# Optimization experiments

Measured on AMD Instinct MI355X. Metric: run time of the kernel, lower is better.

The kernel has to match this reference:

```python
import jax, jax.numpy as jnp
import numpy as np

NUM_HEADS = 16
HEAD_DIM = 64
EMBED_DIM = NUM_HEADS * HEAD_DIM  # 1024


def setup_inputs() -> dict:
    key = jax.random.key(0)
    k1, k2, k3 = jax.random.split(key, 3)
    B, T, C = 4, 2048, EMBED_DIM
    x = jax.random.normal(k1, (B, T, C), dtype=jnp.float32)
    # Linear weights stored [in, out] so y = x @ W (== torch x @ W.T with torch layout)
    w_qkv = jax.random.normal(k2, (C, 3 * C), dtype=jnp.float32) * (1.0 / np.sqrt(C))
    w_out = jax.random.normal(k3, (C, C), dtype=jnp.float32) * (1.0 / np.sqrt(C))
    return {"x": x, "w_qkv": w_qkv, "w_out": w_out}


def reference(x, w_qkv, w_out):
    B, T, C = x.shape
    H, D = NUM_HEADS, HEAD_DIM
    scale = 1.0 / jnp.sqrt(jnp.asarray(D, dtype=x.dtype))

    qkv = x @ w_qkv  # [B, T, 3C]
    q, k, v = jnp.split(qkv, 3, axis=-1)

    def split_heads(t):
        return t.reshape(B, T, H, D).transpose(0, 2, 1, 3)  # [B, H, T, D]

    q, k, v = split_heads(q), split_heads(k), split_heads(v)

    scores = jnp.einsum("bhqd,bhkd->bhqk", q, k) * scale  # [B, H, T, T]
    causal = jnp.tril(jnp.ones((T, T), dtype=bool))
    scores = jnp.where(causal, scores, -jnp.inf)
    weights = jax.nn.softmax(scores, axis=-1)
    out = jnp.einsum("bhqk,bhkd->bhqd", weights, v)  # [B, H, T, D]
    out = out.transpose(0, 2, 1, 3).reshape(B, T, C)
    return out @ w_out
```

## Files before the change

kernel.cpp:

```cpp
#include <hip/hip_runtime.h>

typedef __attribute__((ext_vector_type(8))) short bf16x8;
typedef __attribute__((ext_vector_type(4))) float f32x4;
typedef __attribute__((ext_vector_type(8))) unsigned short u16x8;

#define USHORT unsigned short

__device__ __forceinline__ USHORT f2bf(float f){
  unsigned int u = __builtin_bit_cast(unsigned int, f);
  u = (u + 0x7FFFu + ((u >> 16) & 1u)) >> 16;
  return (USHORT)u;
}

__device__ __forceinline__ void gl_lds16(const void* g, void* l){
  __builtin_amdgcn_global_load_lds((const __attribute__((address_space(1))) void*)g,
                                   (__attribute__((address_space(3))) void*)l, 16, 0, 0);
}

__global__ __launch_bounds__(256) void cvt_x(const float* __restrict__ x,
                                             USHORT* __restrict__ xb){
  int i = blockIdx.x * 256 + threadIdx.x;
  const float4* p = (const float4*)x;
  float4 a = p[i*2], b = p[i*2+1];
  u16x8 v;
  v[0]=f2bf(a.x); v[1]=f2bf(a.y); v[2]=f2bf(a.z); v[3]=f2bf(a.w);
  v[4]=f2bf(b.x); v[5]=f2bf(b.y); v[6]=f2bf(b.z); v[7]=f2bf(b.w);
  ((u16x8*)xb)[i] = v;
}

__global__ __launch_bounds__(256) void transpose_f32_bf16(const float* __restrict__ src,
                                                          USHORT* __restrict__ dst,
                                                          int rows, int cols){
  __shared__ USHORT t[32][33];
  int x0 = blockIdx.x * 32, y0 = blockIdx.y * 32;
  int tx = threadIdx.x, ty = threadIdx.y;
  #pragma unroll
  for (int i=0;i<4;i++)
    t[ty+i*8][tx] = f2bf(src[(size_t)(y0+ty+i*8)*cols + x0+tx]);
  __syncthreads();
  #pragma unroll
  for (int i=0;i<4;i++)
    dst[(size_t)(x0+ty+i*8)*rows + y0+tx] = t[tx][ty+i*8];
}

__global__ __launch_bounds__(256) void transpose_v(const USHORT* __restrict__ V,
                                                   USHORT* __restrict__ VT){
  __shared__ USHORT t[32][33];
  int bh = blockIdx.z;
  const USHORT* src = V + (size_t)bh*2048*64;
  USHORT* dst = VT + (size_t)bh*64*2048;
  int x0 = blockIdx.x * 32;
  int y0 = blockIdx.y * 32;
  int tx = threadIdx.x, ty = threadIdx.y;
  #pragma unroll
  for (int i=0;i<4;i++)
    t[ty+i*8][tx] = src[(size_t)(y0+ty+i*8)*64 + x0+tx];
  __syncthreads();
  #pragma unroll
  for (int i=0;i<4;i++)
    dst[(size_t)(x0+ty+i*8)*2048 + y0+tx] = t[tx][ty+i*8];
}

template<int EPI>
__global__ __launch_bounds__(256) void gemm_bt(
    const USHORT* __restrict__ A, const USHORT* __restrict__ Bt,
    float* __restrict__ Cf,
    USHORT* __restrict__ Qo, USHORT* __restrict__ Ko, USHORT* __restrict__ Vo,
    int M, int N, int K)
{
  __shared__ USHORT As[128*32];
  __shared__ USHORT Bs[128*32];
  const int tid = threadIdx.x;
  const int lane = tid & 63, li = lane & 15, g = lane >> 4;
  const int wv = tid >> 6, wr = wv >> 1, wc = wv & 1;
  const int m0 = blockIdx.y * 128, n0 = blockIdx.x * 128;

  f32x4 acc[4][4];
  #pragma unroll
  for (int m=0;m<4;m++)
    #pragma unroll
    for (int n=0;n<4;n++) acc[m][n] = (f32x4){0.f,0.f,0.f,0.f};

  for (int kk = 0; kk < K; kk += 32){
    __syncthreads();
    #pragma unroll
    for (int it=0; it<2; ++it){
      int c = it*256 + tid;
      int row = c >> 2, sl = c & 3;
      gl_lds16(A  + (size_t)(m0+row)*K + kk + sl*8, &As[c*8]);
      gl_lds16(Bt + (size_t)(n0+row)*K + kk + sl*8, &Bs[c*8]);
    }
    __syncthreads();
    bf16x8 af[4], bfr[4];
    #pragma unroll
    for (int m=0;m<4;m++) af[m]  = *(const bf16x8*)&As[(wr*64+m*16+li)*32 + g*8];
    #pragma unroll
    for (int n=0;n<4;n++) bfr[n] = *(const bf16x8*)&Bs[(wc*64+n*16+li)*32 + g*8];
    #pragma unroll
    for (int m=0;m<4;m++)
      #pragma unroll
      for (int n=0;n<4;n++)
        acc[m][n] = __builtin_amdgcn_mfma_f32_16x16x32_bf16(af[m], bfr[n], acc[m][n], 0,0,0);
  }

  if (EPI == 0){
    #pragma unroll
    for (int m=0;m<4;m++)
      #pragma unroll
      for (int n=0;n<4;n++){
        int col  = n0 + wc*64 + n*16 + li;
        int rowb = m0 + wr*64 + m*16 + g*4;
        #pragma unroll
        for (int r=0;r<4;r++)
          Cf[(size_t)(rowb+r)*N + col] = acc[m][n][r];
      }
  } else {
    #pragma unroll
    for (int m=0;m<4;m++)
      #pragma unroll
      for (int n=0;n<4;n++){
        int col = n0 + wc*64 + n*16 + li;
        int which = col >> 10, hd = col & 1023, h = hd >> 6, d = hd & 63;
        USHORT* dst = (which==0) ? Qo : ((which==1) ? Ko : Vo);
        float sc = (which==0) ? 0.125f : 1.0f;
        int rowb = m0 + wr*64 + m*16 + g*4;
        #pragma unroll
        for (int r=0;r<4;r++){
          int grow = rowb + r;
          int b = grow >> 11, t = grow & 2047;
          dst[((size_t)(b*16+h)*2048 + t)*64 + d] = f2bf(acc[m][n][r]*sc);
        }
      }
  }
}

__global__ __launch_bounds__(256) void attn_kern(
    const USHORT* __restrict__ Q, const USHORT* __restrict__ Kc,
    const USHORT* __restrict__ VT, USHORT* __restrict__ Aout)
{
  __shared__ USHORT Kl[128*64];
  __shared__ USHORT Vl[64*128];
  __shared__ USHORT Pl[128*128];
  const int qt = blockIdx.x, bh = blockIdx.y;
  const int q0 = qt * 128;
  const int tid = threadIdx.x, lane = tid & 63, li = lane & 15, g = lane >> 4;
  const int wv = tid >> 6;
  const USHORT* Qb = Q  + (size_t)bh*2048*64;
  const USHORT* Kb = Kc + (size_t)bh*2048*64;
  const USHORT* Vb = VT + (size_t)bh*64*2048;

  bf16x8 aq[2][2];
  #pragma unroll
  for (int m=0;m<2;m++)
    #pragma unroll
    for (int ks=0;ks<2;ks++){
      int row = q0 + wv*32 + m*16 + li;
      aq[m][ks] = *(const bf16x8*)&Qb[(size_t)row*64 + ks*32 + g*8];
    }

  f32x4 o[2][4];
  float mrun[2][4], lrun[2][4];
  #pragma unroll
  for (int m=0;m<2;m++){
    #pragma unroll
    for (int n=0;n<4;n++) o[m][n] = (f32x4){0.f,0.f,0.f,0.f};
    #pragma unroll
    for (int r=0;r<4;r++){ mrun[m][r] = -1e30f; lrun[m][r] = 0.f; }
  }

  const int nkt = qt + 1;
  for (int kt = 0; kt < nkt; ++kt){
    __syncthreads();
    #pragma unroll
    for (int it=0; it<4; ++it){
      int c = it*256 + tid;
      { int row = c >> 3, sl = c & 7, gs = sl ^ (row & 7);
        gl_lds16(Kb + ((size_t)(kt*128+row))*64 + gs*8, &Kl[c*8]); }
      { int row = c >> 4, sl = c & 15, gs = sl ^ (row & 15);
        gl_lds16(Vb + (size_t)row*2048 + kt*128 + gs*8, &Vl[c*8]); }
    }
    __syncthreads();

    f32x4 s[2][8];
    #pragma unroll
    for (int m=0;m<2;m++)
      #pragma unroll
      for (int nf=0;nf<8;nf++){
        f32x4 z = (f32x4){0.f,0.f,0.f,0.f};
        #pragma unroll
        for (int ks=0;ks<2;ks++){
          int key = nf*16 + li;
          int addr = (key*128 + ks*64 + g*16) ^ ((key & 7) << 4);
          bf16x8 bk = *(const bf16x8*)((const char*)Kl + addr);
          z = __builtin_amdgcn_mfma_f32_16x16x32_bf16(aq[m][ks], bk, z, 0,0,0);
        }
        s[m][nf] = z;
      }

    if (kt == qt){
      #pragma unroll
      for (int m=0;m<2;m++){
        int rowb = q0 + wv*32 + m*16 + g*4;
        #pragma unroll
        for (int nf=0;nf<8;nf++){
          int col = kt*128 + nf*16 + li;
          #pragma unroll
          for (int r=0;r<4;r++)
            if (col > rowb + r) s[m][nf][r] = -1e30f;
        }
      }
    }

    #pragma unroll
    for (int m=0;m<2;m++){
      #pragma unroll
      for (int r=0;r<4;r++){
        float v = s[m][0][r];
        #pragma unroll
        for (int nf=1;nf<8;nf++) v = fmaxf(v, s[m][nf][r]);
        #pragma unroll
        for (int d=1;d<16;d<<=1) v = fmaxf(v, __shfl_xor(v, d, 64));
        float mnew = fmaxf(mrun[m][r], v);
        float scale = __expf(mrun[m][r] - mnew);
        float psum = 0.f;
        #pragma unroll
        for (int nf=0;nf<8;nf++){
          float p = __expf(s[m][nf][r] - mnew);
          s[m][nf][r] = p;
          psum += p;
        }
        #pragma unroll
        for (int d=1;d<16;d<<=1) psum += __shfl_xor(psum, d, 64);
        lrun[m][r] = lrun[m][r]*scale + psum;
        mrun[m][r] = mnew;
        #pragma unroll
        for (int nd=0;nd<4;nd++) o[m][nd][r] *= scale;
      }
      #pragma unroll
      for (int nf=0;nf<8;nf++)
        #pragma unroll
        for (int r=0;r<4;r++){
          int prow = wv*32 + m*16 + g*4 + r;
          int pcol = nf*16 + li;
          int addr = (prow*256 + pcol*2) ^ ((prow & 15) << 4);
          *(USHORT*)((char*)Pl + addr) = f2bf(s[m][nf][r]);
        }
    }
    __syncthreads();

    #pragma unroll
    for (int m=0;m<2;m++)
      #pragma unroll
      for (int nd=0;nd<4;nd++){
        #pragma unroll
        for (int ks=0;ks<4;ks++){
          int prow = wv*32 + m*16 + li;
          int paddr = (prow*256 + ks*64 + g*16) ^ ((prow & 15) << 4);
          bf16x8 pa = *(const bf16x8*)((const char*)Pl + paddr);
          int d = nd*16 + li;
          int vaddr = (d*256 + ks*64 + g*16) ^ ((d & 15) << 4);
          bf16x8 vb = *(const bf16x8*)((const char*)Vl + vaddr);
          o[m][nd] = __builtin_amdgcn_mfma_f32_16x16x32_bf16(pa, vb, o[m][nd], 0,0,0);
        }
      }
  }

  const int b = bh >> 4, h = bh & 15;
  #pragma unroll
  for (int m=0;m<2;m++)
    #pragma unroll
    for (int nd=0;nd<4;nd++)
      #pragma unroll
      for (int r=0;r<4;r++){
        int t = q0 + wv*32 + m*16 + g*4 + r;
        int d = nd*16 + li;
        float val = o[m][nd][r] / lrun[m][r];
        Aout[((size_t)(b*2048 + t))*1024 + h*64 + d] = f2bf(val);
      }
}

extern "C" void kernel_launch(void* const* d_in, const int* in_sizes, int n_in,
                              void* d_out, int out_size, void* d_ws, size_t ws_size,
                              hipStream_t stream) {
  const float* x     = (const float*)d_in[0];
  const float* w_qkv = (const float*)d_in[1];
  const float* w_out = (const float*)d_in[2];
  float* out = (float*)d_out;
  char* ws = (char*)d_ws;

  USHORT* xb    = (USHORT*)(ws);
  USHORT* wqkvT = (USHORT*)(ws + 16777216);
  USHORT* woutT = (USHORT*)(ws + 23068672);
  USHORT* Qb    = (USHORT*)(ws + 25165824);
  USHORT* Kb    = (USHORT*)(ws + 41943040);
  USHORT* Vb    = (USHORT*)(ws + 58720256);
  USHORT* VT    = xb;
  USHORT* Aout  = Vb;

  cvt_x<<<4096, 256, 0, stream>>>(x, xb);
  transpose_f32_bf16<<<dim3(96,32), dim3(32,8), 0, stream>>>(w_qkv, wqkvT, 1024, 3072);
  transpose_f32_bf16<<<dim3(32,32), dim3(32,8), 0, stream>>>(w_out, woutT, 1024, 1024);
  gemm_bt<1><<<dim3(24,64), 256, 0, stream>>>(xb, wqkvT, nullptr, Qb, Kb, Vb, 8192, 3072, 1024);
  transpose_v<<<dim3(2,64,64), dim3(32,8), 0, stream>>>(Vb, VT);
  attn_kern<<<dim3(16,64), 256, 0, stream>>>(Qb, Kb, VT, Aout);
  gemm_bt<0><<<dim3(8,64), 256, 0, stream>>>(Aout, woutT, out, nullptr, nullptr, nullptr, 8192, 1024, 1024);
}
```

Before: 476.1 us.

## Read K/V directly from global memory with per-wave P buffers and reversed tile order

The attention kernel no longer stages K and V tiles through shared memory with block-wide barriers. Each wave now loads K and V fragments straight from global memory (relying on cache), uses 64-key tiles, and keeps P in a private per-wave LDS slice so no __syncthreads is needed. Query tiles are also launched in reverse order so the longest causal rows start first. The trade-off is redundant global and L2 traffic, since all four waves fetch the same K/V, in exchange for removing sync stalls and freeing LDS for higher occupancy.

```diff
diff --git a/kernel.cpp b/kernel.cpp
--- a/kernel.cpp
+++ b/kernel.cpp
@@ -138,16 +138,16 @@
     const USHORT* __restrict__ Q, const USHORT* __restrict__ Kc,
     const USHORT* __restrict__ VT, USHORT* __restrict__ Aout)
 {
-  __shared__ USHORT Kl[128*64];
-  __shared__ USHORT Vl[64*128];
-  __shared__ USHORT Pl[128*128];
-  const int qt = blockIdx.x, bh = blockIdx.y;
+  __shared__ USHORT Pl[4][32*64];
+  const int qt = 15 - blockIdx.x;
+  const int bh = blockIdx.y;
   const int q0 = qt * 128;
   const int tid = threadIdx.x, lane = tid & 63, li = lane & 15, g = lane >> 4;
   const int wv = tid >> 6;
   const USHORT* Qb = Q  + (size_t)bh*2048*64;
   const USHORT* Kb = Kc + (size_t)bh*2048*64;
   const USHORT* Vb = VT + (size_t)bh*64*2048;
+  char* pw = (char*)&Pl[wv][0];
 
   bf16x8 aq[2][2];
   #pragma unroll
@@ -168,42 +168,31 @@
     for (int r=0;r<4;r++){ mrun[m][r] = -1e30f; lrun[m][r] = 0.f; }
   }
 
-  const int nkt = qt + 1;
+  const int nkt = 2*qt + 2;
   for (int kt = 0; kt < nkt; ++kt){
-    __syncthreads();
-    #pragma unroll
-    for (int it=0; it<4; ++it){
-      int c = it*256 + tid;
-      { int row = c >> 3, sl = c & 7, gs = sl ^ (row & 7);
-        gl_lds16(Kb + ((size_t)(kt*128+row))*64 + gs*8, &Kl[c*8]); }
-      { int row = c >> 4, sl = c & 15, gs = sl ^ (row & 15);
-        gl_lds16(Vb + (size_t)row*2048 + kt*128 + gs*8, &Vl[c*8]); }
-    }
-    __syncthreads();
-
-    f32x4 s[2][8];
+    const USHORT* Kt = Kb + (size_t)kt*64*64;
+
+    f32x4 s[2][4];
     #pragma unroll
     for (int m=0;m<2;m++)
       #pragma unroll
-      for (int nf=0;nf<8;nf++){
+      for (int nf=0;nf<4;nf++){
         f32x4 z = (f32x4){0.f,0.f,0.f,0.f};
         #pragma unroll
         for (int ks=0;ks<2;ks++){
-          int key = nf*16 + li;
-          int addr = (key*128 + ks*64 + g*16) ^ ((key & 7) << 4);
-          bf16x8 bk = *(const bf16x8*)((const char*)Kl + addr);
+          bf16x8 bk = *(const bf16x8*)&Kt[(size_t)(nf*16+li)*64 + ks*32 + g*8];
           z = __builtin_amdgcn_mfma_f32_16x16x32_bf16(aq[m][ks], bk, z, 0,0,0);
         }
         s[m][nf] = z;
       }
 
-    if (kt == qt){
+    if (kt >= 2*qt){
       #pragma unroll
       for (int m=0;m<2;m++){
         int rowb = q0 + wv*32 + m*16 + g*4;
         #pragma unroll
-        for (int nf=0;nf<8;nf++){
-          int col = kt*128 + nf*16 + li;
+        for (int nf=0;nf<4;nf++){
+          int col = kt*64 + nf*16 + li;
           #pragma unroll
           for (int r=0;r<4;r++)
             if (col > rowb + r) s[m][nf][r] = -1e30f;
@@ -217,14 +206,14 @@
       for (int r=0;r<4;r++){
         float v = s[m][0][r];
         #pragma unroll
-        for (int nf=1;nf<8;nf++) v = fmaxf(v, s[m][nf][r]);
+        for (int nf=1;nf<4;nf++) v = fmaxf(v, s[m][nf][r]);
         #pragma unroll
         for (int d=1;d<16;d<<=1) v = fmaxf(v, __shfl_xor(v, d, 64));
         float mnew = fmaxf(mrun[m][r], v);
         float scale = __expf(mrun[m][r] - mnew);
         float psum = 0.f;
         #pragma unroll
-        for (int nf=0;nf<8;nf++){
+        for (int nf=0;nf<4;nf++){
           float p = __expf(s[m][nf][r] - mnew);
           s[m][nf][r] = p;
           psum += p;
@@ -237,32 +226,33 @@
         for (int nd=0;nd<4;nd++) o[m][nd][r] *= scale;
       }
       #pragma unroll
-      for (int nf=0;nf<8;nf++)
+      for (int nf=0;nf<4;nf++)
         #pragma unroll
         for (int r=0;r<4;r++){
-          int prow = wv*32 + m*16 + g*4 + r;
-          int pcol = nf*16 + li;
-          int addr = (prow*256 + pcol*2) ^ ((prow & 15) << 4);
-          *(USHORT*)((char*)Pl + addr) = f2bf(s[m][nf][r]);
-        }
-    }
-    __syncthreads();
-
-    #pragma unroll
-    for (int m=0;m<2;m++)
-      #pragma unroll
-      for (int nd=0;nd<4;nd++){
-        #pragma unroll
-        for (int ks=0;ks<4;ks++){
-          int prow = wv*32 + m*16 + li;
-          int paddr = (prow*256 + ks*64 + g*16) ^ ((prow & 15) << 4);
-          bf16x8 pa = *(const bf16x8*)((const char*)Pl + paddr);
-          int d = nd*16 + li;
-          int vaddr = (d*256 + ks*64 + g*16) ^ ((d & 15) << 4);
-          bf16x8 vb = *(const bf16x8*)((const char*)Vl + vaddr);
+          int q = m*16 + g*4 + r;
+          int key = nf*16 + li;
+          int addr = q*128 + ((key*2) ^ ((q & 7) << 4));
+          *(USHORT*)(pw + addr) = f2bf(s[m][nf][r]);
+        }
+    }
+
+    asm volatile("s_waitcnt lgkmcnt(0)" ::: "memory");
+    __builtin_amdgcn_sched_barrier(0);
+
+    #pragma unroll
+    for (int m=0;m<2;m++){
+      int prow = m*16 + li;
+      int xorv = (prow & 7) << 4;
+      #pragma unroll
+      for (int ks=0;ks<2;ks++){
+        bf16x8 pa = *(const bf16x8*)(pw + prow*128 + ((ks*64 + g*16) ^ xorv));
+        #pragma unroll
+        for (int nd=0;nd<4;nd++){
+          bf16x8 vb = *(const bf16x8*)&Vb[(size_t)(nd*16+li)*2048 + kt*64 + ks*32 + g*8];
           o[m][nd] = __builtin_amdgcn_mfma_f32_16x16x32_bf16(pa, vb, o[m][nd], 0,0,0);
         }
       }
+    }
   }
 
   const int b = bh >> 4, h = bh & 15;
```

After: 448.8 us. 5.7% less time.
